# Kernel optimization log

Measured on AMD Instinct MI355X. Metric: run time of the kernel, lower is better.

Reference implementation:

```python
import jax, jax.numpy as jnp
import numpy as np


def _sobel_filters():
    # fil is the 3x3 smoothing kernel [[1,2,1],[2,4,2],[1,2,1]]
    fil = np.array([[1, 2, 1], [2, 4, 2], [1, 2, 1]], dtype=np.float32)
    fx = np.zeros((3, 3, 3), dtype=np.float32)
    fx[0, :, :] = fil
    fx[2, :, :] = -fil
    fy = np.zeros((3, 3, 3), dtype=np.float32)
    fy[:, 0, :] = fil
    fy[:, 2, :] = -fil
    fz = np.zeros((3, 3, 3), dtype=np.float32)
    fz[:, :, 0] = fil
    fz[:, :, 2] = -fil
    # Stack the three fixed (non-learned) filters as 3 output channels: [O=3, I=1, 3,3,3]
    return jnp.asarray(np.stack([fx, fy, fz])[:, None])


_FILT = _sobel_filters()
_DN = ('NCDHW', 'OIDHW', 'NCDHW')


def _grad3d(v):
    # v: [N,1,D,H,W] -> [N,3,D,H,W], padding=1 == SAME for 3x3x3 stride 1
    return jax.lax.conv_general_dilated(
        v, _FILT.astype(v.dtype), window_strides=(1, 1, 1),
        padding='SAME', dimension_numbers=_DN)


def setup_inputs() -> dict:
    key = jax.random.key(0)
    k1, k2 = jax.random.split(key)
    shape = (2, 1, 160, 192, 224)
    x = jax.random.normal(k1, shape, dtype=jnp.float32)
    y = jax.random.normal(k2, shape, dtype=jnp.float32)
    return {"x": x, "y": y}


def reference(x, y):
    gx = _grad3d(x)  # [N,3,D,H,W]
    gy = _grad3d(y)
    d2 = (gx - gy) ** 2
    # sum over the 3 directions of the per-direction MSE
    return jnp.sum(jnp.mean(d2, axis=(0, 2, 3, 4)))
```

## Files before the change

kernel.cpp:

```cpp
#include <hip/hip_runtime.h>


#define N_  2
#define D_  160
#define H_  192
#define W_  224

#define TW  64
#define TH  12
#define TD  8

constexpr int LROWS = TH + 2;
constexpr int LCW   = 18;
constexpr int LCOLS = LCW * 4;
constexpr int NCHUNK = LROWS * LCW;
constexpr int PS = H_ * W_;
constexpr float SCALE = 1.0f / ((float)N_ * D_ * H_ * W_);

__global__ __launch_bounds__(256, 6)
void grad_loss_kernel(const float* __restrict__ x, const float* __restrict__ y,
                      float* __restrict__ out) {
    __shared__ float plane[2][LROWS][LCOLS];
    __shared__ float wsum[4];

    const int tx  = threadIdx.x;
    const int ty  = threadIdx.y;
    const int tid = ty * 64 + tx;

    const int w0 = blockIdx.x * TW;
    const int h0 = blockIdx.y * TH;
    const int nchunks = D_ / TD;
    const int n  = blockIdx.z / nchunks;
    const int d0 = (blockIdx.z % nchunks) * TD;

    const size_t base = (size_t)n * D_ * PS;
    const bool active = (w0 + tx) < W_;

    const bool stager = tid < NCHUNK;
    const int srow = tid / LCW;
    const int sci  = tid - srow * LCW;
    const int gh   = h0 - 1 + srow;
    const int gw0  = w0 - 4 + 4 * sci;
    const bool sok = stager && (unsigned)gh < (unsigned)H_ &&
                     (unsigned)gw0 < (unsigned)W_;
    const float* px = x + base + (size_t)gh * W_ + gw0;
    const float* py = y + base + (size_t)gh * W_ + gw0;
    float* const ldst0 = &plane[0][0][0] + (srow * LCOLS + 4 * sci);
    float* const ldst1 = &plane[1][0][0] + (srow * LCOLS + 4 * sci);

    float a0[3], a1[3], a2[3], b0[3], b1[3], b2[3];
    float acc = 0.f;
    const int rbase = 3 * ty;

    float4 rx = make_float4(0.f, 0.f, 0.f, 0.f), ry = rx;
    if (sok && d0 - 1 >= 0) {
        rx = *(const float4*)(px + (size_t)(d0 - 1) * PS);
        ry = *(const float4*)(py + (size_t)(d0 - 1) * PS);
    }
    if (stager)
        *(float4*)ldst0 = make_float4(rx.x - ry.x, rx.y - ry.y,
                                      rx.z - ry.z, rx.w - ry.w);
    rx = make_float4(0.f, 0.f, 0.f, 0.f); ry = rx;
    if (sok) {
        rx = *(const float4*)(px + (size_t)d0 * PS);
        ry = *(const float4*)(py + (size_t)d0 * PS);
    }

    for (int it = 0; it <= TD + 1; ++it) {
        __syncthreads();
        float (*buf)[LCOLS] = plane[it & 1];

        float sw[5], gww[5];
        #pragma unroll
        for (int r = 0; r < 5; ++r) {
            float a = buf[rbase + r][tx + 3];
            float b = buf[rbase + r][tx + 4];
            float c = buf[rbase + r][tx + 5];
            sw[r]  = a + 2.f * b + c;
            gww[r] = a - c;
        }
        float n0[3], n1[3], n2[3];
        #pragma unroll
        for (int j = 0; j < 3; ++j) {
            n0[j] = sw[j] + 2.f * sw[j + 1] + sw[j + 2];
            n1[j] = sw[j] - sw[j + 2];
            n2[j] = gww[j] + 2.f * gww[j + 1] + gww[j + 2];
        }

        if (it >= 2 && active) {
            #pragma unroll
            for (int j = 0; j < 3; ++j) {
                float gx = a0[j] - n0[j];
                float gy = a1[j] + 2.f * b1[j] + n1[j];
                float gz = a2[j] + 2.f * b2[j] + n2[j];
                acc = fmaf(gx, gx, acc);
                acc = fmaf(gy, gy, acc);
                acc = fmaf(gz, gz, acc);
            }
        }

        #pragma unroll
        for (int j = 0; j < 3; ++j) {
            a0[j] = b0[j]; a1[j] = b1[j]; a2[j] = b2[j];
            b0[j] = n0[j]; b1[j] = n1[j]; b2[j] = n2[j];
        }

        if (it < TD + 1) {
            float4 nx = make_float4(0.f, 0.f, 0.f, 0.f), ny = nx;
            if (it < TD) {
                int q = d0 + it + 1;
                if (sok && q < D_) {
                    nx = *(const float4*)(px + (size_t)q * PS);
                    ny = *(const float4*)(py + (size_t)q * PS);
                }
            }
            if (stager) {
                float* dst = (it & 1) ? ldst0 : ldst1;
                *(float4*)dst = make_float4(rx.x - ry.x, rx.y - ry.y,
                                            rx.z - ry.z, rx.w - ry.w);
            }
            rx = nx; ry = ny;
        }
    }

    #pragma unroll
    for (int off = 32; off > 0; off >>= 1)
        acc += __shfl_down(acc, off, 64);
    if (tx == 0) wsum[ty] = acc;
    __syncthreads();
    if (tid == 0) {
        float s = (wsum[0] + wsum[1]) + (wsum[2] + wsum[3]);
        atomicAdd(out, s * SCALE);
    }
}

extern "C" void kernel_launch(void* const* d_in, const int* in_sizes, int n_in,
                              void* d_out, int out_size, void* d_ws, size_t ws_size,
                              hipStream_t stream) {
    const float* x = (const float*)d_in[0];
    const float* y = (const float*)d_in[1];
    float* out = (float*)d_out;

    hipMemsetAsync(out, 0, sizeof(float), stream);

    dim3 block(TW, 256 / TW);
    dim3 grid((W_ + TW - 1) / TW,
              H_ / TH,
              N_ * (D_ / TD));
    grad_loss_kernel<<<grid, block, 0, stream>>>(x, y, out);
}
```

Measured before the change: 152.0 us.

## Stage two depth planes per barrier and fully unroll the depth loop

```diff
diff --git a/kernel.cpp b/kernel.cpp
--- a/kernel.cpp
+++ b/kernel.cpp
@@ -5,6 +5,7 @@
 #define D_  160
 #define H_  192
 #define W_  224
+#define PS  (H_ * W_)
 
 #define TW  64
 #define TH  12
@@ -14,13 +15,12 @@
 constexpr int LCW   = 18;
 constexpr int LCOLS = LCW * 4;
 constexpr int NCHUNK = LROWS * LCW;
-constexpr int PS = H_ * W_;
 constexpr float SCALE = 1.0f / ((float)N_ * D_ * H_ * W_);
 
-__global__ __launch_bounds__(256, 6)
+__global__ __launch_bounds__(256, 8)
 void grad_loss_kernel(const float* __restrict__ x, const float* __restrict__ y,
                       float* __restrict__ out) {
-    __shared__ float plane[2][LROWS][LCOLS];
+    __shared__ float plane[2][2][LROWS][LCOLS];
     __shared__ float wsum[4];
 
     const int tx  = threadIdx.x;
@@ -30,10 +30,10 @@
     const int w0 = blockIdx.x * TW;
     const int h0 = blockIdx.y * TH;
     const int nchunks = D_ / TD;
-    const int n  = blockIdx.z / nchunks;
+    const int nb = blockIdx.z / nchunks;
     const int d0 = (blockIdx.z % nchunks) * TD;
 
-    const size_t base = (size_t)n * D_ * PS;
+    const size_t base = (size_t)nb * ((size_t)D_ * PS);
     const bool active = (w0 + tx) < W_;
 
     const bool stager = tid < NCHUNK;
@@ -45,87 +45,76 @@
                      (unsigned)gw0 < (unsigned)W_;
     const float* px = x + base + (size_t)gh * W_ + gw0;
     const float* py = y + base + (size_t)gh * W_ + gw0;
-    float* const ldst0 = &plane[0][0][0] + (srow * LCOLS + 4 * sci);
-    float* const ldst1 = &plane[1][0][0] + (srow * LCOLS + 4 * sci);
+    const int loff = srow * LCOLS + 4 * sci;
 
     float a0[3], a1[3], a2[3], b0[3], b1[3], b2[3];
     float acc = 0.f;
     const int rbase = 3 * ty;
 
-    float4 rx = make_float4(0.f, 0.f, 0.f, 0.f), ry = rx;
-    if (sok && d0 - 1 >= 0) {
-        rx = *(const float4*)(px + (size_t)(d0 - 1) * PS);
-        ry = *(const float4*)(py + (size_t)(d0 - 1) * PS);
-    }
-    if (stager)
-        *(float4*)ldst0 = make_float4(rx.x - ry.x, rx.y - ry.y,
-                                      rx.z - ry.z, rx.w - ry.w);
-    rx = make_float4(0.f, 0.f, 0.f, 0.f); ry = rx;
-    if (sok) {
-        rx = *(const float4*)(px + (size_t)d0 * PS);
-        ry = *(const float4*)(py + (size_t)d0 * PS);
-    }
+    const float4 z4 = make_float4(0.f, 0.f, 0.f, 0.f);
 
-    for (int it = 0; it <= TD + 1; ++it) {
+    #pragma unroll
+    for (int it = 0; it < (TD + 2) / 2; ++it) {
+        const int p0 = d0 - 1 + 2 * it;
+        const int p1 = p0 + 1;
+
+        float4 xA = z4, yA = z4, xB = z4, yB = z4;
+        const bool okA = sok && (p0 >= 0);
+        const bool okB = sok && (p1 < D_);
+        if (okA) { xA = *(const float4*)(px + (size_t)p0 * PS);
+                   yA = *(const float4*)(py + (size_t)p0 * PS); }
+        if (okB) { xB = *(const float4*)(px + (size_t)p1 * PS);
+                   yB = *(const float4*)(py + (size_t)p1 * PS); }
+        if (stager) {
+            *(float4*)(&plane[it & 1][0][0][0] + loff) =
+                make_float4(xA.x - yA.x, xA.y - yA.y, xA.z - yA.z, xA.w - yA.w);
+            *(float4*)(&plane[it & 1][1][0][0] + loff) =
+                make_float4(xB.x - yB.x, xB.y - yB.y, xB.z - yB.z, xB.w - yB.w);
+        }
         __syncthreads();
-        float (*buf)[LCOLS] = plane[it & 1];
 
-        float sw[5], gww[5];
         #pragma unroll
-        for (int r = 0; r < 5; ++r) {
-            float a = buf[rbase + r][tx + 3];
-            float b = buf[rbase + r][tx + 4];
-            float c = buf[rbase + r][tx + 5];
-            sw[r]  = a + 2.f * b + c;
-            gww[r] = a - c;
-        }
-        float n0[3], n1[3], n2[3];
-        #pragma unroll
-        for (int j = 0; j < 3; ++j) {
-            n0[j] = sw[j] + 2.f * sw[j + 1] + sw[j + 2];
-            n1[j] = sw[j] - sw[j + 2];
-            n2[j] = gww[j] + 2.f * gww[j + 1] + gww[j + 2];
-        }
-
-        if (it >= 2 && active) {
+        for (int s = 0; s < 2; ++s) {
+            const float (*buf)[LCOLS] = plane[it & 1][s];
+            float sw[5], gww[5];
+            #pragma unroll
+            for (int r = 0; r < 5; ++r) {
+                float a = buf[rbase + r][tx + 3];
+                float b = buf[rbase + r][tx + 4];
+                float c = buf[rbase + r][tx + 5];
+                sw[r]  = a + 2.f * b + c;
+                gww[r] = a - c;
+            }
+            float n0[3], n1[3], n2[3];
             #pragma unroll
             for (int j = 0; j < 3; ++j) {
-                float gx = a0[j] - n0[j];
-                float gy = a1[j] + 2.f * b1[j] + n1[j];
-                float gz = a2[j] + 2.f * b2[j] + n2[j];
-                acc = fmaf(gx, gx, acc);
-                acc = fmaf(gy, gy, acc);
-                acc = fmaf(gz, gz, acc);
+                n0[j] = sw[j] + 2.f * sw[j + 1] + sw[j + 2];
+                n1[j] = sw[j] - sw[j + 2];
+                n2[j] = gww[j] + 2.f * gww[j + 1] + gww[j + 2];
             }
-        }
 
-        #pragma unroll
-        for (int j = 0; j < 3; ++j) {
-            a0[j] = b0[j]; a1[j] = b1[j]; a2[j] = b2[j];
-            b0[j] = n0[j]; b1[j] = n1[j]; b2[j] = n2[j];
-        }
-
-        if (it < TD + 1) {
-            float4 nx = make_float4(0.f, 0.f, 0.f, 0.f), ny = nx;
-            if (it < TD) {
-                int q = d0 + it + 1;
-                if (sok && q < D_) {
-                    nx = *(const float4*)(px + (size_t)q * PS);
-                    ny = *(const float4*)(py + (size_t)q * PS);
+            if (it >= 1 && active) {
+                #pragma unroll
+                for (int j = 0; j < 3; ++j) {
+                    float gx = a0[j] - n0[j];
+                    float gy = a1[j] + 2.f * b1[j] + n1[j];
+                    float gz = a2[j] + 2.f * b2[j] + n2[j];
+                    acc = fmaf(gx, gx, acc);
+                    acc = fmaf(gy, gy, acc);
+                    acc = fmaf(gz, gz, acc);
                 }
             }
-            if (stager) {
-                float* dst = (it & 1) ? ldst0 : ldst1;
-                *(float4*)dst = make_float4(rx.x - ry.x, rx.y - ry.y,
-                                            rx.z - ry.z, rx.w - ry.w);
+            #pragma unroll
+            for (int j = 0; j < 3; ++j) {
+                a0[j] = b0[j]; a1[j] = b1[j]; a2[j] = b2[j];
+                b0[j] = n0[j]; b1[j] = n1[j]; b2[j] = n2[j];
             }
-            rx = nx; ry = ny;
         }
     }
 
     #pragma unroll
     for (int off = 32; off > 0; off >>= 1)
-        acc += __shfl_down(acc, off, 64);
+        acc += __shfl_xor(acc, off, 64);
     if (tx == 0) wsum[ty] = acc;
     __syncthreads();
     if (tid == 0) {
```

Measured after the change: 151.7 us. No clear change (-0.2%).
